# Optimization experiments

Hardware: AMD Instinct MI355X
Metric: run time of the kernel (lower is better)

Reference implementation:

```python
import jax, jax.numpy as jnp
import numpy as np

N, E = 100000, 1600000
IN_C, HID_C, OUT_C = 128, 64, 40


def setup_inputs() -> dict:
    key = jax.random.key(0)
    ks = jax.random.split(key, 8)
    s = lambda fan_in: 1.0 / np.sqrt(fan_in)
    return {
        "x": jax.random.normal(ks[0], (N, IN_C), dtype=jnp.float32),
        "edge_index": jax.random.randint(ks[1], (2, E), 0, N, dtype=jnp.int64),
        # SAGEConv layer 1: lin_l (on aggregated neighbors, with bias) + lin_r (root, no bias)
        "W_l1": jax.random.uniform(ks[2], (IN_C, HID_C), jnp.float32, -s(IN_C), s(IN_C)),
        "b_l1": jnp.zeros((HID_C,), jnp.float32),
        "W_r1": jax.random.uniform(ks[3], (IN_C, HID_C), jnp.float32, -s(IN_C), s(IN_C)),
        # SAGEConv layer 2
        "W_l2": jax.random.uniform(ks[4], (HID_C, OUT_C), jnp.float32, -s(HID_C), s(HID_C)),
        "b_l2": jnp.zeros((OUT_C,), jnp.float32),
        "W_r2": jax.random.uniform(ks[5], (HID_C, OUT_C), jnp.float32, -s(HID_C), s(HID_C)),
    }


def _sage_conv(x, src, dst, W_l, b_l, W_r, n_nodes):
    # mean-aggregate neighbor features: scatter-add x[src] onto dst, divide by degree
    agg = jax.ops.segment_sum(x[src], dst, num_segments=n_nodes)  # [N, F]
    deg = jax.ops.segment_sum(jnp.ones((src.shape[0],), x.dtype), dst, num_segments=n_nodes)
    mean = agg / jnp.maximum(deg, 1.0)[:, None]
    return mean @ W_l + b_l + x @ W_r


def reference(x, edge_index, W_l1, b_l1, W_r1, W_l2, b_l2, W_r2):
    src, dst = edge_index[0], edge_index[1]  # messages flow src -> dst
    # eval mode: dropout is identity
    hid = _sage_conv(x, src, dst, W_l1, b_l1, W_r1, N)
    hid = jax.nn.relu(hid)
    out = _sage_conv(hid, src, dst, W_l2, b_l2, W_r2, N)
    return jax.nn.log_softmax(out, axis=1)
```

## Files before the change

### kernel.cpp

```cpp
#include <hip/hip_runtime.h>
#include <hip/hip_bf16.h>

#define N_NODES 100000
#define E_EDGES 1600000
#define IN_C 128
#define HID_C 64
#define OUT_C 40

#define NBUCK 196
#define BCAP 9216
#define B1_EPT 16
#define B1_CHUNK (256 * B1_EPT)
#define B1_GRID ((E_EDGES + B1_CHUNK - 1) / B1_CHUNK)

typedef unsigned short ushort_t;
typedef unsigned int uint_t;
typedef unsigned char uchar_t;
typedef __attribute__((ext_vector_type(8))) short bf16x8;
typedef __attribute__((ext_vector_type(4))) float f32x4;
typedef __attribute__((ext_vector_type(2))) float f32x2;

__device__ __forceinline__ float bfu2f(ushort_t u) {
    return __uint_as_float(((uint_t)u) << 16);
}
__device__ __forceinline__ ushort_t f2bfu(float f) {
    uint_t u = __float_as_uint(f);
    return (ushort_t)((u + 0x7FFFu + ((u >> 16) & 1u)) >> 16);
}
__device__ __forceinline__ uchar_t f2fp8(float f) {
    int p = __builtin_amdgcn_cvt_pk_fp8_f32(f, f, 0, false);
    return (uchar_t)(p & 0xff);
}

__global__ __launch_bounds__(256) void k_bucket(const int* __restrict__ src, const int* __restrict__ dst,
                                                int* __restrict__ bcur, int* __restrict__ bucket) {
    __shared__ int cnt[NBUCK];
    __shared__ int base[NBUCK];
    const int t = threadIdx.x;
    const int e0 = blockIdx.x * B1_CHUNK;

    for (int i = t; i < NBUCK; i += 256) cnt[i] = 0;
    __syncthreads();

    int myp[B1_EPT];
    int myb[B1_EPT];
#pragma unroll
    for (int j = 0; j < B1_EPT; ++j) {
        int e = e0 + t + j * 256;
        if (e < E_EDGES) {
            int d = dst[e];
            myp[j] = src[e] | ((d & 511) << 17);
            myb[j] = d >> 9;
            atomicAdd(&cnt[myb[j]], 1);
        } else {
            myb[j] = -1;
        }
    }
    __syncthreads();
    for (int i = t; i < NBUCK; i += 256) {
        base[i] = atomicAdd(&bcur[i], cnt[i]);
        cnt[i] = 0;
    }
    __syncthreads();
#pragma unroll
    for (int j = 0; j < B1_EPT; ++j) {
        if (myb[j] >= 0) {
            int b = myb[j];
            int loc = atomicAdd(&cnt[b], 1);
            int pos = base[b] + loc;
            if (pos < BCAP) bucket[(size_t)b * BCAP + pos] = myp[j];
        }
    }
}

__global__ __launch_bounds__(256) void k_scanS(const int* __restrict__ bcur, int* __restrict__ bbase,
                                               int* __restrict__ rowptr) {
    __shared__ int tmp[256];
    int t = threadIdx.x;
    int v = (t < NBUCK) ? min(bcur[t], BCAP) : 0;
    tmp[t] = v;
    __syncthreads();
    for (int off = 1; off < 256; off <<= 1) {
        int a = (t >= off) ? tmp[t - off] : 0;
        __syncthreads();
        tmp[t] += a;
        __syncthreads();
    }
    if (t < NBUCK) bbase[t] = tmp[t] - v;
    if (t == 0) rowptr[N_NODES] = tmp[255];
}

__global__ __launch_bounds__(256) void k_csr(const int* __restrict__ bucket, const int* __restrict__ bcur,
                                             const int* __restrict__ bbase,
                                             int* __restrict__ rowptr, int* __restrict__ csr) {
    __shared__ int hist[512];
    __shared__ int sc[2][512];
    __shared__ int cur[512];
    __shared__ int csrbuf[BCAP];
    const int t = threadIdx.x;
    const int b = blockIdx.x;
    const int n0 = b << 9;
    const int nb = min(512, N_NODES - n0);
    const int sz = min(bcur[b], BCAP);
    const int cbase = bbase[b];
    const int* bdata = bucket + (size_t)b * BCAP;

    for (int i = t; i < 512; i += 256) hist[i] = 0;
    __syncthreads();
    for (int i = t; i < sz; i += 256) {
        int p = bdata[i];
        atomicAdd(&hist[p >> 17], 1);
    }
    __syncthreads();
    for (int i = t; i < 512; i += 256) sc[0][i] = hist[i];
    __syncthreads();
    int pp = 0;
    for (int off = 1; off < 512; off <<= 1) {
        for (int i = t; i < 512; i += 256)
            sc[1 - pp][i] = sc[pp][i] + ((i >= off) ? sc[pp][i - off] : 0);
        __syncthreads();
        pp ^= 1;
    }
    for (int i = t; i < 512; i += 256) {
        int exc = sc[pp][i] - hist[i];
        cur[i] = exc;
        if (i < nb) rowptr[n0 + i] = cbase + exc;
    }
    __syncthreads();
    for (int i = t; i < sz; i += 256) {
        int p = bdata[i];
        int pos = atomicAdd(&cur[p >> 17], 1);
        csrbuf[pos] = p & 0x1FFFF;
    }
    __syncthreads();
    for (int i = t; i < sz; i += 256)
        csr[cbase + i] = csrbuf[i];
}

__global__ __launch_bounds__(256) void k_wprep(const float* __restrict__ Wl1, const float* __restrict__ Wr1,
                                               const float* __restrict__ Wl2, const float* __restrict__ Wr2,
                                               ushort_t* __restrict__ Wt1, ushort_t* __restrict__ Wt2) {
    int i = blockIdx.x * 256 + threadIdx.x;
    if (i < 128 * 128) {
        int n = i >> 7, k = i & 127;
        float v = (n < 64) ? Wl1[k * 64 + n] : Wr1[k * 64 + (n - 64)];
        Wt1[n * 128 + k] = f2bfu(v);
    }
    if (i < 80 * 64) {
        int n = i >> 6, k = i & 63;
        float v = (n < 40) ? Wl2[k * 40 + n] : Wr2[k * 40 + (n - 40)];
        Wt2[n * 64 + k] = f2bfu(v);
    }
}

__global__ __launch_bounds__(256) void k_gemm1(const float* __restrict__ x,
                                               const ushort_t* __restrict__ Wt,
                                               uchar_t* __restrict__ h1l,
                                               float* __restrict__ h1r) {
    __shared__ ushort_t xs[64 * 136];
    __shared__ ushort_t wsm[128 * 136];
    const int t = threadIdx.x;
    const int row_base = blockIdx.x * 64;

    for (int i = t; i < 128 * 16; i += 256) {
        int n = i >> 4, seg = i & 15;
        uint4 v = *(const uint4*)(Wt + n * 128 + seg * 8);
        *(uint4*)(wsm + n * 136 + seg * 8) = v;
    }
    for (int i = t; i < 64 * 32; i += 256) {
        int row = i >> 5, seg = i & 31;
        int gr = row_base + row;
        float4 v = make_float4(0.f, 0.f, 0.f, 0.f);
        if (gr < N_NODES) v = *(const float4*)(x + (size_t)gr * IN_C + seg * 4);
        ushort4 u;
        u.x = f2bfu(v.x); u.y = f2bfu(v.y); u.z = f2bfu(v.z); u.w = f2bfu(v.w);
        *(ushort4*)(xs + row * 136 + seg * 4) = u;
    }
    __syncthreads();

    const int wv = t >> 6, lane = t & 63;
    const int m = lane & 15, quad = lane >> 4;
    const int m0 = wv * 16;

    bf16x8 a[4];
#pragma unroll
    for (int kk = 0; kk < 4; ++kk)
        a[kk] = *(const bf16x8*)(xs + (m0 + m) * 136 + kk * 32 + quad * 8);

    f32x4 acc[8];
#pragma unroll
    for (int nt = 0; nt < 8; ++nt) acc[nt] = (f32x4){0.f, 0.f, 0.f, 0.f};

#pragma unroll
    for (int nt = 0; nt < 8; ++nt) {
#pragma unroll
        for (int kk = 0; kk < 4; ++kk) {
            bf16x8 b = *(const bf16x8*)(wsm + (nt * 16 + m) * 136 + kk * 32 + quad * 8);
            acc[nt] = __builtin_amdgcn_mfma_f32_16x16x32_bf16(a[kk], b, acc[nt], 0, 0, 0);
        }
    }

    const int grow_base = row_base + m0 + quad * 4;
#pragma unroll
    for (int r = 0; r < 4; ++r) {
        int grow = grow_base + r;
        if (grow < N_NODES) {
#pragma unroll
            for (int nt = 0; nt < 4; ++nt)
                h1l[(size_t)grow * HID_C + nt * 16 + m] = f2fp8(acc[nt][r]);
#pragma unroll
            for (int nt = 4; nt < 8; ++nt)
                h1r[(size_t)grow * HID_C + (nt - 4) * 16 + m] = acc[nt][r];
        }
    }
}

__global__ __launch_bounds__(256) void k_agg1(const int* __restrict__ rowptr, const int* __restrict__ csr,
                                              const uchar_t* __restrict__ h1l, const float* __restrict__ h1r,
                                              const float* __restrict__ b1, ushort_t* __restrict__ hid) {
    int row = (blockIdx.x * 256 + threadIdx.x) >> 6;
    int lane = threadIdx.x & 63;
    if (row >= N_NODES) return;
    int start = rowptr[row];
    int end = rowptr[row + 1];
    const int slot = lane >> 3;
    const int part = lane & 7;
    float acc[8] = {0.f, 0.f, 0.f, 0.f, 0.f, 0.f, 0.f, 0.f};

    for (int base = start; base < end; base += 8) {
        int e = base + slot;
        int ee = min(e, end - 1);
        int s = csr[ee];
        uint2 u = *(const uint2*)(h1l + ((size_t)s << 6) + part * 8);
        if (e >= end) { u.x = 0u; u.y = 0u; }
        f32x2 f;
        f = __builtin_amdgcn_cvt_pk_f32_fp8(u.x, false); acc[0] += f.x; acc[1] += f.y;
        f = __builtin_amdgcn_cvt_pk_f32_fp8(u.x, true);  acc[2] += f.x; acc[3] += f.y;
        f = __builtin_amdgcn_cvt_pk_f32_fp8(u.y, false); acc[4] += f.x; acc[5] += f.y;
        f = __builtin_amdgcn_cvt_pk_f32_fp8(u.y, true);  acc[6] += f.x; acc[7] += f.y;
    }
#pragma unroll
    for (int off = 8; off <= 32; off <<= 1)
#pragma unroll
        for (int j = 0; j < 8; ++j)
            acc[j] += __shfl_xor(acc[j], off);

    if (slot == 0) {
        float inv = __builtin_amdgcn_rcpf(fmaxf((float)(end - start), 1.0f));
        size_t bi = (size_t)row * HID_C + part * 8;
        float4 r0 = *(const float4*)(h1r + bi);
        float4 r1 = *(const float4*)(h1r + bi + 4);
        float4 bb0 = *(const float4*)(b1 + part * 8);
        float4 bb1 = *(const float4*)(b1 + part * 8 + 4);
        ushort_t o[8];
        o[0] = f2bfu(fmaxf(acc[0] * inv + r0.x + bb0.x, 0.f));
        o[1] = f2bfu(fmaxf(acc[1] * inv + r0.y + bb0.y, 0.f));
        o[2] = f2bfu(fmaxf(acc[2] * inv + r0.z + bb0.z, 0.f));
        o[3] = f2bfu(fmaxf(acc[3] * inv + r0.w + bb0.w, 0.f));
        o[4] = f2bfu(fmaxf(acc[4] * inv + r1.x + bb1.x, 0.f));
        o[5] = f2bfu(fmaxf(acc[5] * inv + r1.y + bb1.y, 0.f));
        o[6] = f2bfu(fmaxf(acc[6] * inv + r1.z + bb1.z, 0.f));
        o[7] = f2bfu(fmaxf(acc[7] * inv + r1.w + bb1.w, 0.f));
        *(uint4*)(hid + bi) = *(const uint4*)o;
    }
}

__global__ __launch_bounds__(256) void k_gemm2(const ushort_t* __restrict__ hid,
                                               const ushort_t* __restrict__ Wt,
                                               uchar_t* __restrict__ h2l,
                                               float* __restrict__ h2r) {
    __shared__ ushort_t hs[64 * 72];
    __shared__ ushort_t wsm[80 * 72];
    const int t = threadIdx.x;
    const int row_base = blockIdx.x * 64;

    for (int i = t; i < 80 * 8; i += 256) {
        int n = i >> 3, seg = i & 7;
        uint4 v = *(const uint4*)(Wt + n * 64 + seg * 8);
        *(uint4*)(wsm + n * 72 + seg * 8) = v;
    }
    for (int i = t; i < 64 * 8; i += 256) {
        int row = i >> 3, seg = i & 7;
        int gr = row_base + row;
        uint4 v = make_uint4(0u, 0u, 0u, 0u);
        if (gr < N_NODES) v = *(const uint4*)(hid + (size_t)gr * HID_C + seg * 8);
        *(uint4*)(hs + row * 72 + seg * 8) = v;
    }
    __syncthreads();

    const int wv = t >> 6, lane = t & 63;
    const int m = lane & 15, quad = lane >> 4;
    const int m0 = wv * 16;

    bf16x8 a[2];
#pragma unroll
    for (int kk = 0; kk < 2; ++kk)
        a[kk] = *(const bf16x8*)(hs + (m0 + m) * 72 + kk * 32 + quad * 8);

    f32x4 acc[5];
#pragma unroll
    for (int nt = 0; nt < 5; ++nt) acc[nt] = (f32x4){0.f, 0.f, 0.f, 0.f};

#pragma unroll
    for (int nt = 0; nt < 5; ++nt) {
#pragma unroll
        for (int kk = 0; kk < 2; ++kk) {
            bf16x8 b = *(const bf16x8*)(wsm + (nt * 16 + m) * 72 + kk * 32 + quad * 8);
            acc[nt] = __builtin_amdgcn_mfma_f32_16x16x32_bf16(a[kk], b, acc[nt], 0, 0, 0);
        }
    }

    const int grow_base = row_base + m0 + quad * 4;
#pragma unroll
    for (int r = 0; r < 4; ++r) {
        int grow = grow_base + r;
        if (grow < N_NODES) {
#pragma unroll
            for (int nt = 0; nt < 5; ++nt) {
                int col = nt * 16 + m;
                float v = acc[nt][r];
                if (col < OUT_C) h2l[(size_t)grow * 64 + col] = f2fp8(v);
                else             h2r[(size_t)grow * OUT_C + (col - OUT_C)] = v;
            }
        }
    }
}

__global__ __launch_bounds__(256) void k_agg2(const int* __restrict__ rowptr, const int* __restrict__ csr,
                                              const uchar_t* __restrict__ h2l, const float* __restrict__ h2r,
                                              const float* __restrict__ b2, float* __restrict__ out) {
    int row = (blockIdx.x * 256 + threadIdx.x) >> 6;
    int lane = threadIdx.x & 63;
    if (row >= N_NODES) return;
    int start = rowptr[row];
    int end = rowptr[row + 1];
    const int slot = lane >> 3;
    const int part = lane & 7;
    const bool pvalid = part < 5;
    float acc[8] = {0.f, 0.f, 0.f, 0.f, 0.f, 0.f, 0.f, 0.f};

    for (int base = start; base < end; base += 8) {
        int e = base + slot;
        int ee = min(e, end - 1);
        int s = csr[ee];
        uint2 u = *(const uint2*)(h2l + ((size_t)s << 6) + part * 8);
        if (e >= end || !pvalid) { u.x = 0u; u.y = 0u; }
        f32x2 f;
        f = __builtin_amdgcn_cvt_pk_f32_fp8(u.x, false); acc[0] += f.x; acc[1] += f.y;
        f = __builtin_amdgcn_cvt_pk_f32_fp8(u.x, true);  acc[2] += f.x; acc[3] += f.y;
        f = __builtin_amdgcn_cvt_pk_f32_fp8(u.y, false); acc[4] += f.x; acc[5] += f.y;
        f = __builtin_amdgcn_cvt_pk_f32_fp8(u.y, true);  acc[6] += f.x; acc[7] += f.y;
    }
#pragma unroll
    for (int off = 8; off <= 32; off <<= 1)
#pragma unroll
        for (int j = 0; j < 8; ++j)
            acc[j] += __shfl_xor(acc[j], off);

    const bool fin = (slot == 0) && pvalid;
    float inv = __builtin_amdgcn_rcpf(fmaxf((float)(end - start), 1.0f));
    float v[8];
    if (fin) {
        size_t bi = (size_t)row * OUT_C + part * 8;
        float4 r0 = *(const float4*)(h2r + bi);
        float4 r1 = *(const float4*)(h2r + bi + 4);
        float4 bb0 = *(const float4*)(b2 + part * 8);
        float4 bb1 = *(const float4*)(b2 + part * 8 + 4);
        v[0] = acc[0] * inv + r0.x + bb0.x;
        v[1] = acc[1] * inv + r0.y + bb0.y;
        v[2] = acc[2] * inv + r0.z + bb0.z;
        v[3] = acc[3] * inv + r0.w + bb0.w;
        v[4] = acc[4] * inv + r1.x + bb1.x;
        v[5] = acc[5] * inv + r1.y + bb1.y;
        v[6] = acc[6] * inv + r1.z + bb1.z;
        v[7] = acc[7] * inv + r1.w + bb1.w;
    } else {
#pragma unroll
        for (int j = 0; j < 8; ++j) v[j] = -1e30f;
    }
    float pm = v[0];
#pragma unroll
    for (int j = 1; j < 8; ++j) pm = fmaxf(pm, v[j]);
#pragma unroll
    for (int off = 1; off <= 4; off <<= 1) pm = fmaxf(pm, __shfl_xor(pm, off));
    float es = 0.f;
#pragma unroll
    for (int j = 0; j < 8; ++j) es += expf(v[j] - pm);
#pragma unroll
    for (int off = 1; off <= 4; off <<= 1) es += __shfl_xor(es, off);
    float ls = logf(es);
    if (fin) {
        size_t bo = (size_t)row * OUT_C + part * 8;
        *(float4*)(out + bo) = make_float4(v[0] - pm - ls, v[1] - pm - ls, v[2] - pm - ls, v[3] - pm - ls);
        *(float4*)(out + bo + 4) = make_float4(v[4] - pm - ls, v[5] - pm - ls, v[6] - pm - ls, v[7] - pm - ls);
    }
}

extern "C" void kernel_launch(void* const* d_in, const int* in_sizes, int n_in,
                              void* d_out, int out_size, void* d_ws, size_t ws_size,
                              hipStream_t stream) {
    const float* x   = (const float*)d_in[0];
    const int*   ei  = (const int*)d_in[1];
    const float* Wl1 = (const float*)d_in[2];
    const float* b1  = (const float*)d_in[3];
    const float* Wr1 = (const float*)d_in[4];
    const float* Wl2 = (const float*)d_in[5];
    const float* b2  = (const float*)d_in[6];
    const float* Wr2 = (const float*)d_in[7];

    size_t u = 0;
    int*      bucket = (int*)d_ws;             u += (size_t)NBUCK * BCAP;
    int*      bcur   = (int*)d_ws + u;         u += NBUCK;
    int*      bbase  = (int*)d_ws + u;         u += NBUCK + 4;
    int*      rowptr = (int*)d_ws + u;         u += N_NODES + 1;
    int*      csr    = (int*)d_ws + u;         u += E_EDGES;
    u = (u + 3) & ~(size_t)3;
    ushort_t* Wt1    = (ushort_t*)((int*)d_ws + u); u += 128 * 128 / 2;
    ushort_t* Wt2    = (ushort_t*)((int*)d_ws + u); u += 80 * 64 / 2;
    uchar_t*  h1l    = (uchar_t*)((int*)d_ws + u);  u += (size_t)N_NODES * HID_C / 4;
    float*    h1r    = (float*)d_ws + u;       u += (size_t)N_NODES * HID_C;
    ushort_t* hid    = (ushort_t*)((int*)d_ws + u); u += (size_t)N_NODES * HID_C / 2;
    uchar_t*  h2l    = (uchar_t*)((int*)d_ws + u);  u += (size_t)N_NODES * 64 / 4;
    float*    h2r    = (float*)d_ws + u;       u += (size_t)N_NODES * OUT_C;
    if (ws_size < u * 4) return;

    hipMemsetAsync(bcur, 0, NBUCK * sizeof(int), stream);

    const int* src = ei;
    const int* dst = ei + E_EDGES;

    k_wprep<<<64, 256, 0, stream>>>(Wl1, Wr1, Wl2, Wr2, Wt1, Wt2);
    k_bucket<<<B1_GRID, 256, 0, stream>>>(src, dst, bcur, bucket);
    k_scanS<<<1, 256, 0, stream>>>(bcur, bbase, rowptr);
    k_csr<<<NBUCK, 256, 0, stream>>>(bucket, bcur, bbase, rowptr, csr);

    k_gemm1<<<(N_NODES + 63) / 64, 256, 0, stream>>>(x, Wt1, h1l, h1r);
    k_agg1<<<N_NODES / 4, 256, 0, stream>>>(rowptr, csr, h1l, h1r, b1, hid);
    k_gemm2<<<(N_NODES + 63) / 64, 256, 0, stream>>>(hid, Wt2, h2l, h2r);
    k_agg2<<<N_NODES / 4, 256, 0, stream>>>(rowptr, csr, h2l, h2r, b2, (float*)d_out);
}
```

Measured before the change: 277.1 us.

## Merge prep and CSR/GEMM1 kernels, store root terms in bf16, split agg tail

Weight prep now shares a launch with edge bucketing. CSR build now shares a launch with GEMM1 as independent block ranges over a shared-memory union. The separate bucket scan is dropped: each CSR block computes its own base with a block reduction over the preceding bucket counts. The root-term intermediates h1r and h2r are stored as bf16 instead of fp32 to halve their traffic, and the aggregation loops get a mask-free main loop with a masked tail. This cuts launches and memory traffic, at the cost of extra bf16 rounding and a larger per-block shared-memory footprint in the fused kernel.

```diff
diff --git a/kernel.cpp b/kernel.cpp
--- a/kernel.cpp
+++ b/kernel.cpp
@@ -12,6 +12,7 @@
 #define B1_EPT 16
 #define B1_CHUNK (256 * B1_EPT)
 #define B1_GRID ((E_EDGES + B1_CHUNK - 1) / B1_CHUNK)
+#define GEMM1_GRID ((N_NODES + 63) / 64)
 
 typedef unsigned short ushort_t;
 typedef unsigned int uint_t;
@@ -32,191 +33,193 @@
     return (uchar_t)(p & 0xff);
 }
 
-__global__ __launch_bounds__(256) void k_bucket(const int* __restrict__ src, const int* __restrict__ dst,
-                                                int* __restrict__ bcur, int* __restrict__ bucket) {
+__global__ __launch_bounds__(256) void k_prep(const int* __restrict__ src, const int* __restrict__ dst,
+                                              int* __restrict__ bcur, int* __restrict__ bucket,
+                                              const float* __restrict__ Wl1, const float* __restrict__ Wr1,
+                                              const float* __restrict__ Wl2, const float* __restrict__ Wr2,
+                                              ushort_t* __restrict__ Wt1, ushort_t* __restrict__ Wt2) {
     __shared__ int cnt[NBUCK];
     __shared__ int base[NBUCK];
     const int t = threadIdx.x;
-    const int e0 = blockIdx.x * B1_CHUNK;
-
-    for (int i = t; i < NBUCK; i += 256) cnt[i] = 0;
-    __syncthreads();
-
-    int myp[B1_EPT];
-    int myb[B1_EPT];
-#pragma unroll
-    for (int j = 0; j < B1_EPT; ++j) {
-        int e = e0 + t + j * 256;
-        if (e < E_EDGES) {
-            int d = dst[e];
-            myp[j] = src[e] | ((d & 511) << 17);
-            myb[j] = d >> 9;
-            atomicAdd(&cnt[myb[j]], 1);
-        } else {
-            myb[j] = -1;
-        }
-    }
-    __syncthreads();
-    for (int i = t; i < NBUCK; i += 256) {
-        base[i] = atomicAdd(&bcur[i], cnt[i]);
-        cnt[i] = 0;
-    }
-    __syncthreads();
-#pragma unroll
-    for (int j = 0; j < B1_EPT; ++j) {
-        if (myb[j] >= 0) {
-            int b = myb[j];
-            int loc = atomicAdd(&cnt[b], 1);
-            int pos = base[b] + loc;
-            if (pos < BCAP) bucket[(size_t)b * BCAP + pos] = myp[j];
-        }
-    }
-}
-
-__global__ __launch_bounds__(256) void k_scanS(const int* __restrict__ bcur, int* __restrict__ bbase,
-                                               int* __restrict__ rowptr) {
-    __shared__ int tmp[256];
-    int t = threadIdx.x;
-    int v = (t < NBUCK) ? min(bcur[t], BCAP) : 0;
-    tmp[t] = v;
-    __syncthreads();
-    for (int off = 1; off < 256; off <<= 1) {
-        int a = (t >= off) ? tmp[t - off] : 0;
-        __syncthreads();
-        tmp[t] += a;
-        __syncthreads();
-    }
-    if (t < NBUCK) bbase[t] = tmp[t] - v;
-    if (t == 0) rowptr[N_NODES] = tmp[255];
-}
-
-__global__ __launch_bounds__(256) void k_csr(const int* __restrict__ bucket, const int* __restrict__ bcur,
-                                             const int* __restrict__ bbase,
-                                             int* __restrict__ rowptr, int* __restrict__ csr) {
-    __shared__ int hist[512];
-    __shared__ int sc[2][512];
-    __shared__ int cur[512];
-    __shared__ int csrbuf[BCAP];
+
+    if (blockIdx.x < B1_GRID) {
+        const int e0 = blockIdx.x * B1_CHUNK;
+        for (int i = t; i < NBUCK; i += 256) cnt[i] = 0;
+        __syncthreads();
+
+        int myp[B1_EPT];
+        int myb[B1_EPT];
+#pragma unroll
+        for (int j = 0; j < B1_EPT; ++j) {
+            int e = e0 + t + j * 256;
+            if (e < E_EDGES) {
+                int d = dst[e];
+                myp[j] = src[e] | ((d & 511) << 17);
+                myb[j] = d >> 9;
+                atomicAdd(&cnt[myb[j]], 1);
+            } else {
+                myb[j] = -1;
+            }
+        }
+        __syncthreads();
+        for (int i = t; i < NBUCK; i += 256) {
+            base[i] = atomicAdd(&bcur[i], cnt[i]);
+            cnt[i] = 0;
+        }
+        __syncthreads();
+#pragma unroll
+        for (int j = 0; j < B1_EPT; ++j) {
+            if (myb[j] >= 0) {
+                int b = myb[j];
+                int loc = atomicAdd(&cnt[b], 1);
+                int pos = base[b] + loc;
+                if (pos < BCAP) bucket[(size_t)b * BCAP + pos] = myp[j];
+            }
+        }
+    } else {
+        int i = (blockIdx.x - B1_GRID) * 256 + t;
+        if (i < 128 * 128) {
+            int n = i >> 7, k = i & 127;
+            float v = (n < 64) ? Wl1[k * 64 + n] : Wr1[k * 64 + (n - 64)];
+            Wt1[n * 128 + k] = f2bfu(v);
+        }
+        if (i < 80 * 64) {
+            int n = i >> 6, k = i & 63;
+            float v = (n < 40) ? Wl2[k * 40 + n] : Wr2[k * 40 + (n - 40)];
+            Wt2[n * 64 + k] = f2bfu(v);
+        }
+    }
+}
+
+struct SmemCsr {
+    int red[256];
+    int hist[512];
+    int sc[2][512];
+    int cur[512];
+    int csrbuf[BCAP];
+};
+struct SmemGemm1 {
+    ushort_t xs[64 * 136];
+    ushort_t wsm[128 * 136];
+};
+union SmemK2 {
+    SmemCsr c;
+    SmemGemm1 g;
+};
+
+__global__ __launch_bounds__(256) void k_csr_gemm1(const int* __restrict__ bucket, const int* __restrict__ bcur,
+                                                   int* __restrict__ rowptr, int* __restrict__ csr,
+                                                   const float* __restrict__ x, const ushort_t* __restrict__ Wt,
+                                                   uchar_t* __restrict__ h1l, ushort_t* __restrict__ h1r) {
+    __shared__ SmemK2 sm;
     const int t = threadIdx.x;
-    const int b = blockIdx.x;
-    const int n0 = b << 9;
-    const int nb = min(512, N_NODES - n0);
-    const int sz = min(bcur[b], BCAP);
-    const int cbase = bbase[b];
-    const int* bdata = bucket + (size_t)b * BCAP;
-
-    for (int i = t; i < 512; i += 256) hist[i] = 0;
-    __syncthreads();
-    for (int i = t; i < sz; i += 256) {
-        int p = bdata[i];
-        atomicAdd(&hist[p >> 17], 1);
-    }
-    __syncthreads();
-    for (int i = t; i < 512; i += 256) sc[0][i] = hist[i];
-    __syncthreads();
-    int pp = 0;
-    for (int off = 1; off < 512; off <<= 1) {
-        for (int i = t; i < 512; i += 256)
-            sc[1 - pp][i] = sc[pp][i] + ((i >= off) ? sc[pp][i - off] : 0);
-        __syncthreads();
-        pp ^= 1;
-    }
-    for (int i = t; i < 512; i += 256) {
-        int exc = sc[pp][i] - hist[i];
-        cur[i] = exc;
-        if (i < nb) rowptr[n0 + i] = cbase + exc;
-    }
-    __syncthreads();
-    for (int i = t; i < sz; i += 256) {
-        int p = bdata[i];
-        int pos = atomicAdd(&cur[p >> 17], 1);
-        csrbuf[pos] = p & 0x1FFFF;
-    }
-    __syncthreads();
-    for (int i = t; i < sz; i += 256)
-        csr[cbase + i] = csrbuf[i];
-}
-
-__global__ __launch_bounds__(256) void k_wprep(const float* __restrict__ Wl1, const float* __restrict__ Wr1,
-                                               const float* __restrict__ Wl2, const float* __restrict__ Wr2,
-                                               ushort_t* __restrict__ Wt1, ushort_t* __restrict__ Wt2) {
-    int i = blockIdx.x * 256 + threadIdx.x;
-    if (i < 128 * 128) {
-        int n = i >> 7, k = i & 127;
-        float v = (n < 64) ? Wl1[k * 64 + n] : Wr1[k * 64 + (n - 64)];
-        Wt1[n * 128 + k] = f2bfu(v);
-    }
-    if (i < 80 * 64) {
-        int n = i >> 6, k = i & 63;
-        float v = (n < 40) ? Wl2[k * 40 + n] : Wr2[k * 40 + (n - 40)];
-        Wt2[n * 64 + k] = f2bfu(v);
-    }
-}
-
-__global__ __launch_bounds__(256) void k_gemm1(const float* __restrict__ x,
-                                               const ushort_t* __restrict__ Wt,
-                                               uchar_t* __restrict__ h1l,
-                                               float* __restrict__ h1r) {
-    __shared__ ushort_t xs[64 * 136];
-    __shared__ ushort_t wsm[128 * 136];
-    const int t = threadIdx.x;
-    const int row_base = blockIdx.x * 64;
-
-    for (int i = t; i < 128 * 16; i += 256) {
-        int n = i >> 4, seg = i & 15;
-        uint4 v = *(const uint4*)(Wt + n * 128 + seg * 8);
-        *(uint4*)(wsm + n * 136 + seg * 8) = v;
-    }
-    for (int i = t; i < 64 * 32; i += 256) {
-        int row = i >> 5, seg = i & 31;
-        int gr = row_base + row;
-        float4 v = make_float4(0.f, 0.f, 0.f, 0.f);
-        if (gr < N_NODES) v = *(const float4*)(x + (size_t)gr * IN_C + seg * 4);
-        ushort4 u;
-        u.x = f2bfu(v.x); u.y = f2bfu(v.y); u.z = f2bfu(v.z); u.w = f2bfu(v.w);
-        *(ushort4*)(xs + row * 136 + seg * 4) = u;
-    }
-    __syncthreads();
-
-    const int wv = t >> 6, lane = t & 63;
-    const int m = lane & 15, quad = lane >> 4;
-    const int m0 = wv * 16;
-
-    bf16x8 a[4];
-#pragma unroll
-    for (int kk = 0; kk < 4; ++kk)
-        a[kk] = *(const bf16x8*)(xs + (m0 + m) * 136 + kk * 32 + quad * 8);
-
-    f32x4 acc[8];
-#pragma unroll
-    for (int nt = 0; nt < 8; ++nt) acc[nt] = (f32x4){0.f, 0.f, 0.f, 0.f};
-
-#pragma unroll
-    for (int nt = 0; nt < 8; ++nt) {
-#pragma unroll
-        for (int kk = 0; kk < 4; ++kk) {
-            bf16x8 b = *(const bf16x8*)(wsm + (nt * 16 + m) * 136 + kk * 32 + quad * 8);
-            acc[nt] = __builtin_amdgcn_mfma_f32_16x16x32_bf16(a[kk], b, acc[nt], 0, 0, 0);
-        }
-    }
-
-    const int grow_base = row_base + m0 + quad * 4;
-#pragma unroll
-    for (int r = 0; r < 4; ++r) {
-        int grow = grow_base + r;
-        if (grow < N_NODES) {
-#pragma unroll
-            for (int nt = 0; nt < 4; ++nt)
-                h1l[(size_t)grow * HID_C + nt * 16 + m] = f2fp8(acc[nt][r]);
-#pragma unroll
-            for (int nt = 4; nt < 8; ++nt)
-                h1r[(size_t)grow * HID_C + (nt - 4) * 16 + m] = acc[nt][r];
+
+    if (blockIdx.x < NBUCK) {
+        const int b = blockIdx.x;
+        const int n0 = b << 9;
+        const int nb = min(512, N_NODES - n0);
+        const int sz = min(bcur[b], BCAP);
+        const int* bdata = bucket + (size_t)b * BCAP;
+
+        int v = (t < b) ? min(bcur[t], BCAP) : 0;
+        sm.c.red[t] = v;
+        __syncthreads();
+        for (int off = 128; off > 0; off >>= 1) {
+            if (t < off) sm.c.red[t] += sm.c.red[t + off];
+            __syncthreads();
+        }
+        const int cbase = sm.c.red[0];
+
+        for (int i = t; i < 512; i += 256) sm.c.hist[i] = 0;
+        __syncthreads();
+        for (int i = t; i < sz; i += 256) {
+            int p = bdata[i];
+            atomicAdd(&sm.c.hist[p >> 17], 1);
+        }
+        __syncthreads();
+        for (int i = t; i < 512; i += 256) sm.c.sc[0][i] = sm.c.hist[i];
+        __syncthreads();
+        int pp = 0;
+        for (int off = 1; off < 512; off <<= 1) {
+            for (int i = t; i < 512; i += 256)
+                sm.c.sc[1 - pp][i] = sm.c.sc[pp][i] + ((i >= off) ? sm.c.sc[pp][i - off] : 0);
+            __syncthreads();
+            pp ^= 1;
+        }
+        for (int i = t; i < 512; i += 256) {
+            int exc = sm.c.sc[pp][i] - sm.c.hist[i];
+            sm.c.cur[i] = exc;
+            if (i < nb) rowptr[n0 + i] = cbase + exc;
+        }
+        __syncthreads();
+        for (int i = t; i < sz; i += 256) {
+            int p = bdata[i];
+            int pos = atomicAdd(&sm.c.cur[p >> 17], 1);
+            sm.c.csrbuf[pos] = p & 0x1FFFF;
+        }
+        __syncthreads();
+        for (int i = t; i < sz; i += 256)
+            csr[cbase + i] = sm.c.csrbuf[i];
+        if (b == NBUCK - 1 && t == 0) rowptr[N_NODES] = cbase + sz;
+    } else {
+        const int row_base = (blockIdx.x - NBUCK) * 64;
+
+        for (int i = t; i < 128 * 16; i += 256) {
+            int n = i >> 4, seg = i & 15;
+            uint4 v = *(const uint4*)(Wt + n * 128 + seg * 8);
+            *(uint4*)(sm.g.wsm + n * 136 + seg * 8) = v;
+        }
+        for (int i = t; i < 64 * 32; i += 256) {
+            int row = i >> 5, seg = i & 31;
+            int gr = row_base + row;
+            float4 v = make_float4(0.f, 0.f, 0.f, 0.f);
+            if (gr < N_NODES) v = *(const float4*)(x + (size_t)gr * IN_C + seg * 4);
+            ushort4 u;
+            u.x = f2bfu(v.x); u.y = f2bfu(v.y); u.z = f2bfu(v.z); u.w = f2bfu(v.w);
+            *(ushort4*)(sm.g.xs + row * 136 + seg * 4) = u;
+        }
+        __syncthreads();
+
+        const int wv = t >> 6, lane = t & 63;
+        const int m = lane & 15, quad = lane >> 4;
+        const int m0 = wv * 16;
+
+        bf16x8 a[4];
+#pragma unroll
+        for (int kk = 0; kk < 4; ++kk)
+            a[kk] = *(const bf16x8*)(sm.g.xs + (m0 + m) * 136 + kk * 32 + quad * 8);
+
+        f32x4 acc[8];
+#pragma unroll
+        for (int nt = 0; nt < 8; ++nt) acc[nt] = (f32x4){0.f, 0.f, 0.f, 0.f};
+
+#pragma unroll
+        for (int nt = 0; nt < 8; ++nt) {
+#pragma unroll
+            for (int kk = 0; kk < 4; ++kk) {
+                bf16x8 b = *(const bf16x8*)(sm.g.wsm + (nt * 16 + m) * 136 + kk * 32 + quad * 8);
+                acc[nt] = __builtin_amdgcn_mfma_f32_16x16x32_bf16(a[kk], b, acc[nt], 0, 0, 0);
+            }
+        }
+
+        const int grow_base = row_base + m0 + quad * 4;
+#pragma unroll
+        for (int r = 0; r < 4; ++r) {
+            int grow = grow_base + r;
+            if (grow < N_NODES) {
+#pragma unroll
+                for (int nt = 0; nt < 4; ++nt)
+                    h1l[(size_t)grow * HID_C + nt * 16 + m] = f2fp8(acc[nt][r]);
+#pragma unroll
+                for (int nt = 4; nt < 8; ++nt)
+                    h1r[(size_t)grow * HID_C + (nt - 4) * 16 + m] = f2bfu(acc[nt][r]);
+            }
         }
     }
 }
 
 __global__ __launch_bounds__(256) void k_agg1(const int* __restrict__ rowptr, const int* __restrict__ csr,
-                                              const uchar_t* __restrict__ h1l, const float* __restrict__ h1r,
+                                              const uchar_t* __restrict__ h1l, const ushort_t* __restrict__ h1r,
                                               const float* __restrict__ b1, ushort_t* __restrict__ hid) {
     int row = (blockIdx.x * 256 + threadIdx.x) >> 6;
     int lane = threadIdx.x & 63;
@@ -227,10 +230,19 @@
     const int part = lane & 7;
     float acc[8] = {0.f, 0.f, 0.f, 0.f, 0.f, 0.f, 0.f, 0.f};
 
-    for (int base = start; base < end; base += 8) {
+    int base = start;
+    for (; base + 8 <= end; base += 8) {
+        int s = csr[base + slot];
+        uint2 u = *(const uint2*)(h1l + ((size_t)s << 6) + part * 8);
+        f32x2 f;
+        f = __builtin_amdgcn_cvt_pk_f32_fp8(u.x, false); acc[0] += f.x; acc[1] += f.y;
+        f = __builtin_amdgcn_cvt_pk_f32_fp8(u.x, true);  acc[2] += f.x; acc[3] += f.y;
+        f = __builtin_amdgcn_cvt_pk_f32_fp8(u.y, false); acc[4] += f.x; acc[5] += f.y;
+        f = __builtin_amdgcn_cvt_pk_f32_fp8(u.y, true);  acc[6] += f.x; acc[7] += f.y;
+    }
+    if (base < end) {
         int e = base + slot;
-        int ee = min(e, end - 1);
-        int s = csr[ee];
+        int s = csr[min(e, end - 1)];
         uint2 u = *(const uint2*)(h1l + ((size_t)s << 6) + part * 8);
         if (e >= end) { u.x = 0u; u.y = 0u; }
         f32x2 f;
@@ -248,19 +260,19 @@
     if (slot == 0) {
         float inv = __builtin_amdgcn_rcpf(fmaxf((float)(end - start), 1.0f));
         size_t bi = (size_t)row * HID_C + part * 8;
-        float4 r0 = *(const float4*)(h1r + bi);
-        float4 r1 = *(const float4*)(h1r + bi + 4);
+        ushort_t rr[8];
+        *(uint4*)rr = *(const uint4*)(h1r + bi);
         float4 bb0 = *(const float4*)(b1 + part * 8);
         float4 bb1 = *(const float4*)(b1 + part * 8 + 4);
         ushort_t o[8];
-        o[0] = f2bfu(fmaxf(acc[0] * inv + r0.x + bb0.x, 0.f));
-        o[1] = f2bfu(fmaxf(acc[1] * inv + r0.y + bb0.y, 0.f));
-        o[2] = f2bfu(fmaxf(acc[2] * inv + r0.z + bb0.z, 0.f));
-        o[3] = f2bfu(fmaxf(acc[3] * inv + r0.w + bb0.w, 0.f));
-        o[4] = f2bfu(fmaxf(acc[4] * inv + r1.x + bb1.x, 0.f));
-        o[5] = f2bfu(fmaxf(acc[5] * inv + r1.y + bb1.y, 0.f));
-        o[6] = f2bfu(fmaxf(acc[6] * inv + r1.z + bb1.z, 0.f));
-        o[7] = f2bfu(fmaxf(acc[7] * inv + r1.w + bb1.w, 0.f));
+        o[0] = f2bfu(fmaxf(acc[0] * inv + bfu2f(rr[0]) + bb0.x, 0.f));
+        o[1] = f2bfu(fmaxf(acc[1] * inv + bfu2f(rr[1]) + bb0.y, 0.f));
+        o[2] = f2bfu(fmaxf(acc[2] * inv + bfu2f(rr[2]) + bb0.z, 0.f));
+        o[3] = f2bfu(fmaxf(acc[3] * inv + bfu2f(rr[3]) + bb0.w, 0.f));
+        o[4] = f2bfu(fmaxf(acc[4] * inv + bfu2f(rr[4]) + bb1.x, 0.f));
+        o[5] = f2bfu(fmaxf(acc[5] * inv + bfu2f(rr[5]) + bb1.y, 0.f));
+        o[6] = f2bfu(fmaxf(acc[6] * inv + bfu2f(rr[6]) + bb1.z, 0.f));
+        o[7] = f2bfu(fmaxf(acc[7] * inv + bfu2f(rr[7]) + bb1.w, 0.f));
         *(uint4*)(hid + bi) = *(const uint4*)o;
     }
 }
@@ -268,7 +280,7 @@
 __global__ __launch_bounds__(256) void k_gemm2(const ushort_t* __restrict__ hid,
                                                const ushort_t* __restrict__ Wt,
                                                uchar_t* __restrict__ h2l,
-                                               float* __restrict__ h2r) {
+                                               ushort_t* __restrict__ h2r) {
     __shared__ ushort_t hs[64 * 72];
     __shared__ ushort_t wsm[80 * 72];
     const int t = threadIdx.x;
@@ -320,14 +332,14 @@
                 int col = nt * 16 + m;
                 float v = acc[nt][r];
                 if (col < OUT_C) h2l[(size_t)grow * 64 + col] = f2fp8(v);
-                else             h2r[(size_t)grow * OUT_C + (col - OUT_C)] = v;
+                else             h2r[(size_t)grow * OUT_C + (col - OUT_C)] = f2bfu(v);
             }
         }
     }
 }
 
 __global__ __launch_bounds__(256) void k_agg2(const int* __restrict__ rowptr, const int* __restrict__ csr,
-                                              const uchar_t* __restrict__ h2l, const float* __restrict__ h2r,
+                                              const uchar_t* __restrict__ h2l, const ushort_t* __restrict__ h2r,
                                               const float* __restrict__ b2, float* __restrict__ out) {
     int row = (blockIdx.x * 256 + threadIdx.x) >> 6;
     int lane = threadIdx.x & 63;
@@ -336,44 +348,53 @@
     int end = rowptr[row + 1];
     const int slot = lane >> 3;
     const int part = lane & 7;
-    const bool pvalid = part < 5;
     float acc[8] = {0.f, 0.f, 0.f, 0.f, 0.f, 0.f, 0.f, 0.f};
 
-    for (int base = start; base < end; base += 8) {
-        int e = base + slot;
-        int ee = min(e, end - 1);
-        int s = csr[ee];
+    int base = start;
+    for (; base + 8 <= end; base += 8) {
+        int s = csr[base + slot];
         uint2 u = *(const uint2*)(h2l + ((size_t)s << 6) + part * 8);
-        if (e >= end || !pvalid) { u.x = 0u; u.y = 0u; }
         f32x2 f;
         f = __builtin_amdgcn_cvt_pk_f32_fp8(u.x, false); acc[0] += f.x; acc[1] += f.y;
         f = __builtin_amdgcn_cvt_pk_f32_fp8(u.x, true);  acc[2] += f.x; acc[3] += f.y;
         f = __builtin_amdgcn_cvt_pk_f32_fp8(u.y, false); acc[4] += f.x; acc[5] += f.y;
         f = __builtin_amdgcn_cvt_pk_f32_fp8(u.y, true);  acc[6] += f.x; acc[7] += f.y;
     }
+    if (base < end) {
+        int e = base + slot;
+        int s = csr[min(e, end - 1)];
+        uint2 u = *(const uint2*)(h2l + ((size_t)s << 6) + part * 8);
+        if (e >= end) { u.x = 0u; u.y = 0u; }
+        f32x2 f;
+        f = __builtin_amdgcn_cvt_pk_f32_fp8(u.x, false); acc[0] += f.x; acc[1] += f.y;
+        f = __builtin_amdgcn_cvt_pk_f32_fp8(u.x, true);  acc[2] += f.x; acc[3] += f.y;
+        f = __builtin_amdgcn_cvt_pk_f32_fp8(u.y, false); acc[4] += f.x; acc[5] += f.y;
+        f = __builtin_amdgcn_cvt_pk_f32_fp8(u.y, true);  acc[6] += f.x; acc[7] += f.y;
+    }
 #pragma unroll
     for (int off = 8; off <= 32; off <<= 1)
 #pragma unroll
         for (int j = 0; j < 8; ++j)
             acc[j] += __shfl_xor(acc[j], off);
 
-    const bool fin = (slot == 0) && pvalid;
+    const bool fin = (slot == 0) && (part < 5);
     float inv = __builtin_amdgcn_rcpf(fmaxf((float)(end - start), 1.0f));
     float v[8];
     if (fin) {
         size_t bi = (size_t)row * OUT_C + part * 8;
-        float4 r0 = *(const float4*)(h2r + bi);
-        float4 r1 = *(const float4*)(h2r + bi + 4);
+        ushort_t rr[8];
+        *(uint2*)&rr[0] = *(const uint2*)(h2r + bi);
+        *(uint2*)&rr[4] = *(const uint2*)(h2r + bi + 4);
         float4 bb0 = *(const float4*)(b2 + part * 8);
         float4 bb1 = *(const float4*)(b2 + part * 8 + 4);
-        v[0] = acc[0] * inv + r0.x + bb0.x;
-        v[1] = acc[1] * inv + r0.y + bb0.y;
-        v[2] = acc[2] * inv + r0.z + bb0.z;
-        v[3] = acc[3] * inv + r0.w + bb0.w;
-        v[4] = acc[4] * inv + r1.x + bb1.x;
-        v[5] = acc[5] * inv + r1.y + bb1.y;
-        v[6] = acc[6] * inv + r1.z + bb1.z;
-        v[7] = acc[7] * inv + r1.w + bb1.w;
+        v[0] = acc[0] * inv + bfu2f(rr[0]) + bb0.x;
+        v[1] = acc[1] * inv + bfu2f(rr[1]) + bb0.y;
+        v[2] = acc[2] * inv + bfu2f(rr[2]) + bb0.z;
+        v[3] = acc[3] * inv + bfu2f(rr[3]) + bb0.w;
+        v[4] = acc[4] * inv + bfu2f(rr[4]) + bb1.x;
+        v[5] = acc[5] * inv + bfu2f(rr[5]) + bb1.y;
+        v[6] = acc[6] * inv + bfu2f(rr[6]) + bb1.z;
+        v[7] = acc[7] * inv + bfu2f(rr[7]) + bb1.w;
     } else {
 #pragma unroll
         for (int j = 0; j < 8; ++j) v[j] = -1e30f;
@@ -410,18 +431,17 @@
 
     size_t u = 0;
     int*      bucket = (int*)d_ws;             u += (size_t)NBUCK * BCAP;
-    int*      bcur   = (int*)d_ws + u;         u += NBUCK;
-    int*      bbase  = (int*)d_ws + u;         u += NBUCK + 4;
+    int*      bcur   = (int*)d_ws + u;         u += NBUCK + 4;
     int*      rowptr = (int*)d_ws + u;         u += N_NODES + 1;
     int*      csr    = (int*)d_ws + u;         u += E_EDGES;
     u = (u + 3) & ~(size_t)3;
     ushort_t* Wt1    = (ushort_t*)((int*)d_ws + u); u += 128 * 128 / 2;
     ushort_t* Wt2    = (ushort_t*)((int*)d_ws + u); u += 80 * 64 / 2;
     uchar_t*  h1l    = (uchar_t*)((int*)d_ws + u);  u += (size_t)N_NODES * HID_C / 4;
-    float*    h1r    = (float*)d_ws + u;       u += (size_t)N_NODES * HID_C;
+    ushort_t* h1r    = (ushort_t*)((int*)d_ws + u); u += (size_t)N_NODES * HID_C / 2;
     ushort_t* hid    = (ushort_t*)((int*)d_ws + u); u += (size_t)N_NODES * HID_C / 2;
     uchar_t*  h2l    = (uchar_t*)((int*)d_ws + u);  u += (size_t)N_NODES * 64 / 4;
-    float*    h2r    = (float*)d_ws + u;       u += (size_t)N_NODES * OUT_C;
+    ushort_t* h2r    = (ushort_t*)((int*)d_ws + u); u += (size_t)N_NODES * OUT_C / 2;
     if (ws_size < u * 4) return;
 
     hipMemsetAsync(bcur, 0, NBUCK * sizeof(int), stream);
@@ -429,13 +449,9 @@
     const int* src = ei;
     const int* dst = ei + E_EDGES;
 
-    k_wprep<<<64, 256, 0, stream>>>(Wl1, Wr1, Wl2, Wr2, Wt1, Wt2);
-    k_bucket<<<B1_GRID, 256, 0, stream>>>(src, dst, bcur, bucket);
-    k_scanS<<<1, 256, 0, stream>>>(bcur, bbase, rowptr);
-    k_csr<<<NBUCK, 256, 0, stream>>>(bucket, bcur, bbase, rowptr, csr);
-
-    k_gemm1<<<(N_NODES + 63) / 64, 256, 0, stream>>>(x, Wt1, h1l, h1r);
+    k_prep<<<B1_GRID + 64, 256, 0, stream>>>(src, dst, bcur, bucket, Wl1, Wr1, Wl2, Wr2, Wt1, Wt2);
+    k_csr_gemm1<<<NBUCK + GEMM1_GRID, 256, 0, stream>>>(bucket, bcur, rowptr, csr, x, Wt1, h1l, h1r);
     k_agg1<<<N_NODES / 4, 256, 0, stream>>>(rowptr, csr, h1l, h1r, b1, hid);
-    k_gemm2<<<(N_NODES + 63) / 64, 256, 0, stream>>>(hid, Wt2, h2l, h2r);
+    k_gemm2<<<GEMM1_GRID, 256, 0, stream>>>(hid, Wt2, h2l, h2r);
     k_agg2<<<N_NODES / 4, 256, 0, stream>>>(rowptr, csr, h2l, h2r, b2, (float*)d_out);
 }
```

After: 264.3 us. -4.6%, faster.
